# Optimization experiments

Measured on AMD Instinct MI355X. Metric: run time of the kernel, lower is better.

The kernel has to match this reference:

```python
import jax, jax.numpy as jnp
import numpy as np

HEAD_SIZE = 2000
TAIL_SAMPLE_SIZE = 100
LOGIT_CLIP = 20.0
B, C, K = 2048, 50000, 10
TAIL_SIZE = C - HEAD_SIZE


def psi(u):
    # logistic surrogate: log(1 + exp(-u))
    return jnp.log1p(jnp.exp(-u))


def setup_inputs() -> dict:
    key = jax.random.key(0)
    k1, k2, k3 = jax.random.split(key, 3)
    logits = jax.random.normal(k1, (B, C), dtype=jnp.float32)
    candidates = jax.random.randint(k2, (B, K), 0, C, dtype=jnp.int64)
    sampled_indices = jax.random.randint(k3, (TAIL_SAMPLE_SIZE,), 0, TAIL_SIZE, dtype=jnp.int64)
    return {"logits": logits, "candidates": candidates, "sampled_indices": sampled_indices}


def reference(logits, candidates, sampled_indices):
    logits = jnp.clip(logits, -LOGIT_CLIP, LOGIT_CLIP)
    batch_size, num_classes = logits.shape
    head_size = min(HEAD_SIZE, num_classes)
    tail_size = max(0, num_classes - head_size)

    valid = candidates >= 0                      # [B, K]
    safe_cand = jnp.where(valid, candidates, 0)  # invalid -> col 0, masked below
    rows = jnp.arange(batch_size)[:, None]       # [B, 1] broadcasts over K

    # y_mask[b, c] = 1 if c in candidate set of row b (scatter-max handles dups)
    y_mask = jnp.zeros((batch_size, num_classes), dtype=logits.dtype)
    y_mask = y_mask.at[rows, safe_cand].max(valid.astype(logits.dtype))

    y_counts = y_mask.sum(axis=1)
    y_card = jnp.maximum(y_counts, 1.0)
    avg_candidate_score = (logits * y_mask).sum(axis=1) / y_card
    term1 = psi(avg_candidate_score)

    # head term: penalize non-candidate head logits
    head_logits = logits[:, :head_size]
    head_mask = y_mask[:, :head_size]  # identical to scatter of (valid & cand < head_size)
    term2 = (psi(-head_logits) * (1.0 - head_mask)).sum(axis=1)

    # sampled tail term
    sampled_tail_logits = logits[:, head_size + sampled_indices]  # [B, S]
    # sampled_is_candidate[b, j] = any_k (candidates[b,k] == head_size + sampled_indices[j])
    sampled_is_candidate = jnp.any(
        (candidates[:, :, None] == (head_size + sampled_indices)[None, None, :]) & valid[:, :, None],
        axis=1,
    )  # [B, S] bool
    tail_scale = float(tail_size) / float(sampled_indices.shape[0])
    term3 = (psi(-sampled_tail_logits) * (~sampled_is_candidate).astype(logits.dtype)).sum(axis=1) * tail_scale

    loss = term1 + term2 + term3
    return loss.mean()
```

## Files before the change

kernel.cpp:

```cpp
#include <hip/hip_runtime.h>

#define HEADN   2000
#define NSAMP   100
#define KC      10
#define CLIPV   20.0f
#define BATCH   2048
#define NCLASS  50000
#define TAILSCL 480.0f

__device__ __forceinline__ float clipf(float x) {
    return fminf(fmaxf(x, -CLIPV), CLIPV);
}

__device__ __forceinline__ float sp(float x) {
    return __logf(1.0f + __expf(x));
}

__global__ __launch_bounds__(256) void row_loss_wave(
        const float* __restrict__ logits,
        const int*   __restrict__ cand,
        const int*   __restrict__ samp,
        float*       __restrict__ row_out)
{
    const int tid  = threadIdx.x;
    const int lane = tid & 63;
    const int row  = blockIdx.x * 4 + (tid >> 6);
    const float* lg = logits + (size_t)row * NCLASS;

    const int cl = (lane < KC) ? cand[row * KC + lane] : -1;
    const int c0 = __shfl(cl, 0), c1 = __shfl(cl, 1), c2 = __shfl(cl, 2),
              c3 = __shfl(cl, 3), c4 = __shfl(cl, 4), c5 = __shfl(cl, 5),
              c6 = __shfl(cl, 6), c7 = __shfl(cl, 7), c8 = __shfl(cl, 8),
              c9 = __shfl(cl, 9);

    float candSum = 0.f, candCnt = 0.f, acc = 0.f;

    if (lane < KC && cl >= 0) {
        bool distinct = true;
        if (lane > 0 && c0 == cl) distinct = false;
        if (lane > 1 && c1 == cl) distinct = false;
        if (lane > 2 && c2 == cl) distinct = false;
        if (lane > 3 && c3 == cl) distinct = false;
        if (lane > 4 && c4 == cl) distinct = false;
        if (lane > 5 && c5 == cl) distinct = false;
        if (lane > 6 && c6 == cl) distinct = false;
        if (lane > 7 && c7 == cl) distinct = false;
        if (lane > 8 && c8 == cl) distinct = false;
        if (distinct) {
            float x = clipf(lg[cl]);
            candSum = x;
            candCnt = 1.f;
            if (cl < HEADN) acc -= sp(x);
        }
    }

    const float4* lg4 = (const float4*)lg;
    #pragma unroll
    for (int k = 0; k < 7; ++k) {
        float4 v = lg4[lane + 64 * k];
        acc += sp(clipf(v.x)) + sp(clipf(v.y)) + sp(clipf(v.z)) + sp(clipf(v.w));
    }
    {
        int i = lane + 448;
        if (i < HEADN / 4) {
            float4 v = lg4[i];
            acc += sp(clipf(v.x)) + sp(clipf(v.y)) + sp(clipf(v.z)) + sp(clipf(v.w));
        }
    }

    {
        const int col = HEADN + samp[lane];
        bool isc = (col == c0) | (col == c1) | (col == c2) | (col == c3) |
                   (col == c4) | (col == c5) | (col == c6) | (col == c7) |
                   (col == c8) | (col == c9);
        if (!isc) acc += TAILSCL * sp(clipf(lg[col]));
    }
    if (lane < NSAMP - 64) {
        const int col = HEADN + samp[lane + 64];
        bool isc = (col == c0) | (col == c1) | (col == c2) | (col == c3) |
                   (col == c4) | (col == c5) | (col == c6) | (col == c7) |
                   (col == c8) | (col == c9);
        if (!isc) acc += TAILSCL * sp(clipf(lg[col]));
    }

    #pragma unroll
    for (int off = 32; off > 0; off >>= 1) {
        candSum += __shfl_xor(candSum, off);
        candCnt += __shfl_xor(candCnt, off);
        acc     += __shfl_xor(acc, off);
    }

    if (lane == 0) {
        float avg = candSum / fmaxf(candCnt, 1.f);
        row_out[row] = sp(-avg) + acc;
    }
}

__global__ __launch_bounds__(256) void mean_kernel(
        const float* __restrict__ row, float* __restrict__ out)
{
    const int tid = threadIdx.x;
    const float4* r4 = (const float4*)row;
    float s = 0.f;
    #pragma unroll
    for (int k = 0; k < BATCH / 4 / 256; ++k) {
        float4 v = r4[tid + 256 * k];
        s += v.x + v.y + v.z + v.w;
    }
    #pragma unroll
    for (int off = 32; off > 0; off >>= 1) s += __shfl_xor(s, off);
    __shared__ float sw[4];
    if ((tid & 63) == 0) sw[tid >> 6] = s;
    __syncthreads();
    if (tid == 0) out[0] = (sw[0] + sw[1] + sw[2] + sw[3]) / (float)BATCH;
}

extern "C" void kernel_launch(void* const* d_in, const int* in_sizes, int n_in,
                              void* d_out, int out_size, void* d_ws, size_t ws_size,
                              hipStream_t stream) {
    const float* logits = (const float*)d_in[0];
    const int*   cand   = (const int*)d_in[1];
    const int*   samp   = (const int*)d_in[2];
    float* row_out = (float*)d_ws;
    float* out     = (float*)d_out;

    row_loss_wave<<<BATCH / 4, 256, 0, stream>>>(logits, cand, samp, row_out);
    mean_kernel<<<1, 256, 0, stream>>>(row_out, out);
}
```

Measured before the change: 15.55 us.

## Split each row across two wavefronts and issue all loads up front

Each row is now handled by two wavefronts instead of one, with each wave covering half of the head columns and half of the tail samples. Per-wave partial sums are combined through shared memory. All global loads (sampled tail, candidates, head float4s) are issued before any compute, and two accumulators are used to raise memory-level parallelism. The mean kernel is shrunk to a single wavefront with no block sync. The trade-off is twice as many blocks plus an added __syncthreads and shared-memory reduction per block.

```diff
diff --git a/kernel.cpp b/kernel.cpp
--- a/kernel.cpp
+++ b/kernel.cpp
@@ -1,6 +1,8 @@
 #include <hip/hip_runtime.h>
 
 #define HEADN   2000
+#define NF4     500
+#define HALF4   250
 #define NSAMP   100
 #define KC      10
 #define CLIPV   20.0f
@@ -16,7 +18,11 @@
     return __logf(1.0f + __expf(x));
 }
 
-__global__ __launch_bounds__(256) void row_loss_wave(
+__device__ __forceinline__ float sp4(float4 v) {
+    return (sp(clipf(v.x)) + sp(clipf(v.y))) + (sp(clipf(v.z)) + sp(clipf(v.w)));
+}
+
+__global__ __launch_bounds__(256) void row_loss_wave2(
         const float* __restrict__ logits,
         const int*   __restrict__ cand,
         const int*   __restrict__ samp,
@@ -24,65 +30,67 @@
 {
     const int tid  = threadIdx.x;
     const int lane = tid & 63;
-    const int row  = blockIdx.x * 4 + (tid >> 6);
+    const int w    = tid >> 6;
+    const int half = w & 1;
+    const int row  = blockIdx.x * 2 + (w >> 1);
     const float* lg = logits + (size_t)row * NCLASS;
 
-    const int cl = (lane < KC) ? cand[row * KC + lane] : -1;
-    const int c0 = __shfl(cl, 0), c1 = __shfl(cl, 1), c2 = __shfl(cl, 2),
-              c3 = __shfl(cl, 3), c4 = __shfl(cl, 4), c5 = __shfl(cl, 5),
-              c6 = __shfl(cl, 6), c7 = __shfl(cl, 7), c8 = __shfl(cl, 8),
-              c9 = __shfl(cl, 9);
+    const bool sAct = lane < 50;
+    const int  scol = HEADN + (sAct ? samp[half * 50 + lane] : 0);
+    const float sval = lg[scol];
 
-    float candSum = 0.f, candCnt = 0.f, acc = 0.f;
+    const int clm = (lane < KC) ? cand[row * KC + lane] : -1;
+    float cval = 0.f;
+    if (half == 0 && clm >= 0) cval = lg[clm];
 
-    if (lane < KC && cl >= 0) {
+    const int c0 = __shfl(clm, 0), c1 = __shfl(clm, 1), c2 = __shfl(clm, 2),
+              c3 = __shfl(clm, 3), c4 = __shfl(clm, 4), c5 = __shfl(clm, 5),
+              c6 = __shfl(clm, 6), c7 = __shfl(clm, 7), c8 = __shfl(clm, 8),
+              c9 = __shfl(clm, 9);
+
+    const float4* lg4 = (const float4*)lg;
+    const int base = half * HALF4;
+    const bool t3 = lane < HALF4 - 192;
+    float4 v0 = lg4[base + lane];
+    float4 v1 = lg4[base + lane + 64];
+    float4 v2 = lg4[base + lane + 128];
+    float4 v3 = lg4[t3 ? (base + lane + 192) : base];
+
+    float candSum = 0.f, candCnt = 0.f;
+    float acc0 = 0.f, acc1 = 0.f;
+
+    acc0 += sp4(v0);
+    acc1 += sp4(v1);
+    acc0 += sp4(v2);
+    if (t3) acc1 += sp4(v3);
+
+    if (sAct) {
+        bool isc = (scol == c0) | (scol == c1) | (scol == c2) | (scol == c3) |
+                   (scol == c4) | (scol == c5) | (scol == c6) | (scol == c7) |
+                   (scol == c8) | (scol == c9);
+        if (!isc) acc0 += TAILSCL * sp(clipf(sval));
+    }
+
+    if (half == 0 && clm >= 0 && lane < KC) {
         bool distinct = true;
-        if (lane > 0 && c0 == cl) distinct = false;
-        if (lane > 1 && c1 == cl) distinct = false;
-        if (lane > 2 && c2 == cl) distinct = false;
-        if (lane > 3 && c3 == cl) distinct = false;
-        if (lane > 4 && c4 == cl) distinct = false;
-        if (lane > 5 && c5 == cl) distinct = false;
-        if (lane > 6 && c6 == cl) distinct = false;
-        if (lane > 7 && c7 == cl) distinct = false;
-        if (lane > 8 && c8 == cl) distinct = false;
+        if (lane > 0 && c0 == clm) distinct = false;
+        if (lane > 1 && c1 == clm) distinct = false;
+        if (lane > 2 && c2 == clm) distinct = false;
+        if (lane > 3 && c3 == clm) distinct = false;
+        if (lane > 4 && c4 == clm) distinct = false;
+        if (lane > 5 && c5 == clm) distinct = false;
+        if (lane > 6 && c6 == clm) distinct = false;
+        if (lane > 7 && c7 == clm) distinct = false;
+        if (lane > 8 && c8 == clm) distinct = false;
         if (distinct) {
-            float x = clipf(lg[cl]);
+            float x = clipf(cval);
             candSum = x;
             candCnt = 1.f;
-            if (cl < HEADN) acc -= sp(x);
+            if (clm < HEADN) acc1 -= sp(x);
         }
     }
 
-    const float4* lg4 = (const float4*)lg;
-    #pragma unroll
-    for (int k = 0; k < 7; ++k) {
-        float4 v = lg4[lane + 64 * k];
-        acc += sp(clipf(v.x)) + sp(clipf(v.y)) + sp(clipf(v.z)) + sp(clipf(v.w));
-    }
-    {
-        int i = lane + 448;
-        if (i < HEADN / 4) {
-            float4 v = lg4[i];
-            acc += sp(clipf(v.x)) + sp(clipf(v.y)) + sp(clipf(v.z)) + sp(clipf(v.w));
-        }
-    }
-
-    {
-        const int col = HEADN + samp[lane];
-        bool isc = (col == c0) | (col == c1) | (col == c2) | (col == c3) |
-                   (col == c4) | (col == c5) | (col == c6) | (col == c7) |
-                   (col == c8) | (col == c9);
-        if (!isc) acc += TAILSCL * sp(clipf(lg[col]));
-    }
-    if (lane < NSAMP - 64) {
-        const int col = HEADN + samp[lane + 64];
-        bool isc = (col == c0) | (col == c1) | (col == c2) | (col == c3) |
-                   (col == c4) | (col == c5) | (col == c6) | (col == c7) |
-                   (col == c8) | (col == c9);
-        if (!isc) acc += TAILSCL * sp(clipf(lg[col]));
-    }
-
+    float acc = acc0 + acc1;
     #pragma unroll
     for (int off = 32; off > 0; off >>= 1) {
         candSum += __shfl_xor(candSum, off);
@@ -90,29 +98,35 @@
         acc     += __shfl_xor(acc, off);
     }
 
-    if (lane == 0) {
-        float avg = candSum / fmaxf(candCnt, 1.f);
-        row_out[row] = sp(-avg) + acc;
+    __shared__ float sS[4], sC[4], sA[4];
+    if (lane == 0) { sS[w] = candSum; sC[w] = candCnt; sA[w] = acc; }
+    __syncthreads();
+    if (tid == 0) {
+        float cs = sS[0] + sS[1], cc = sC[0] + sC[1], a = sA[0] + sA[1];
+        float avg = cs / fmaxf(cc, 1.f);
+        row_out[row] = sp(-avg) + a;
+    }
+    if (tid == 128) {
+        float cs = sS[2] + sS[3], cc = sC[2] + sC[3], a = sA[2] + sA[3];
+        float avg = cs / fmaxf(cc, 1.f);
+        row_out[row] = sp(-avg) + a;
     }
 }
 
-__global__ __launch_bounds__(256) void mean_kernel(
+__global__ __launch_bounds__(64) void mean_kernel(
         const float* __restrict__ row, float* __restrict__ out)
 {
-    const int tid = threadIdx.x;
+    const int lane = threadIdx.x;
     const float4* r4 = (const float4*)row;
     float s = 0.f;
     #pragma unroll
-    for (int k = 0; k < BATCH / 4 / 256; ++k) {
-        float4 v = r4[tid + 256 * k];
-        s += v.x + v.y + v.z + v.w;
+    for (int k = 0; k < BATCH / 4 / 64; ++k) {
+        float4 v = r4[lane + 64 * k];
+        s += (v.x + v.y) + (v.z + v.w);
     }
     #pragma unroll
     for (int off = 32; off > 0; off >>= 1) s += __shfl_xor(s, off);
-    __shared__ float sw[4];
-    if ((tid & 63) == 0) sw[tid >> 6] = s;
-    __syncthreads();
-    if (tid == 0) out[0] = (sw[0] + sw[1] + sw[2] + sw[3]) / (float)BATCH;
+    if (lane == 0) out[0] = s / (float)BATCH;
 }
 
 extern "C" void kernel_launch(void* const* d_in, const int* in_sizes, int n_in,
@@ -124,6 +138,6 @@
     float* row_out = (float*)d_ws;
     float* out     = (float*)d_out;
 
-    row_loss_wave<<<BATCH / 4, 256, 0, stream>>>(logits, cand, samp, row_out);
-    mean_kernel<<<1, 256, 0, stream>>>(row_out, out);
+    row_loss_wave2<<<BATCH / 2, 256, 0, stream>>>(logits, cand, samp, row_out);
+    mean_kernel<<<1, 64, 0, stream>>>(row_out, out);
 }
```

Measured after the change: 16.14 us. 3.8% more time.
